# Performance work log

Hardware: AMD Instinct MI355X
Metric: run time of the kernel (lower is better)

Reference implementation:

```python
import jax, jax.numpy as jnp
import numpy as np

C = 256
CQK = C // 8  # reduction_ratio = 8


def setup_inputs() -> dict:
    key = jax.random.key(0)
    ks = jax.random.split(key, 8)
    B, H, W = 8, 64, 64
    x = jax.random.normal(ks[0], (B, C, H, W), dtype=jnp.float32)
    s_in = 1.0 / np.sqrt(C)
    Wq = jax.random.normal(ks[1], (CQK, C), dtype=jnp.float32) * s_in
    bq = jax.random.normal(ks[2], (CQK,), dtype=jnp.float32) * 0.01
    Wk = jax.random.normal(ks[3], (CQK, C), dtype=jnp.float32) * s_in
    bk = jax.random.normal(ks[4], (CQK,), dtype=jnp.float32) * 0.01
    Wv = jax.random.normal(ks[5], (C, C), dtype=jnp.float32) * s_in
    bv = jax.random.normal(ks[6], (C,), dtype=jnp.float32) * 0.01
    gamma = jax.random.normal(ks[7], (1,), dtype=jnp.float32) * 0.1
    return {"x": x, "Wq": Wq, "bq": bq, "Wk": Wk, "bk": bk,
            "Wv": Wv, "bv": bv, "gamma": gamma}


def reference(x, Wq, bq, Wk, bk, Wv, bv, gamma):
    B, Cc, H, W = x.shape
    N = H * W
    xf = x.reshape(B, Cc, N)  # [B, C, N]
    # 1x1 convs == per-pixel linear maps over channels
    q = jnp.einsum('qc,bcn->bnq', Wq, xf) + bq            # [B, N, Cqk]
    k = jnp.einsum('kc,bcn->bkn', Wk, xf) + bk[None, :, None]  # [B, Cqk, N]
    v = jnp.einsum('vc,bcn->bvn', Wv, xf) + bv[None, :, None]  # [B, C, N]
    # unscaled attention scores, softmax over keys (last dim)
    scores = jax.nn.softmax(jnp.einsum('bnq,bqm->bnm', q, k), axis=-1)  # [B, N, N]
    # out[b,c,n] = sum_m v[b,c,m] * scores[b,n,m]  (torch: value @ scores^T)
    attn = jnp.einsum('bvm,bnm->bvn', v, scores)          # [B, C, N]
    out = gamma[0] * attn.reshape(B, Cc, H, W) + x
    return out
```

## Files before the change

### kernel.cpp

```cpp
#include <hip/hip_runtime.h>

static constexpr int B_   = 8;
static constexpr int C_   = 256;
static constexpr int CQK_ = 32;
static constexpr int N_   = 4096;

typedef __attribute__((ext_vector_type(4)))  float f32x4;
typedef __attribute__((ext_vector_type(16))) float f32x16;
typedef __attribute__((ext_vector_type(8)))  short short8;
typedef __attribute__((ext_vector_type(2)))  unsigned int u32x2;
typedef unsigned short ushort_t;

__device__ inline unsigned short f2bf(float f) {
    unsigned u = __float_as_uint(f);
    return (unsigned short)((u + 0x7FFFu + ((u >> 16) & 1u)) >> 16);
}
__device__ inline unsigned packbf(float lo, float hi) {
    return (unsigned)f2bf(lo) | ((unsigned)f2bf(hi) << 16);
}
__device__ inline unsigned cvtpk(float lo, float hi) {
    unsigned r;
    asm("v_cvt_pk_bf16_f32 %0, %1, %2" : "=v"(r) : "v"(lo), "v"(hi));
    return r;
}
__device__ inline float vexp2(float x) {
    float r;
    asm("v_exp_f32 %0, %1" : "=v"(r) : "v"(x));
    return r;
}
__device__ inline void plswap(unsigned& a, unsigned& b) {
    asm("v_permlane32_swap_b32 %0, %1" : "+v"(a), "+v"(b));
}

__device__ inline int swzbits(int m) {
    return ((m & 3) << 5) | (((m >> 3) & 1) << 4);
}

template <int OFF>
__device__ inline u32x2 tr8(unsigned a) {
    u32x2 d;
    asm volatile("ds_read_b64_tr_b16 %0, %1 offset:%2"
                 : "=v"(d) : "v"(a), "i"(OFF));
    return d;
}

__device__ inline short8 mk8(u32x2 lo, u32x2 hi) {
    union { unsigned u[4]; short8 s; } v;
    v.u[0] = lo.x; v.u[1] = lo.y; v.u[2] = hi.x; v.u[3] = hi.y;
    return v.s;
}
__device__ inline short8 mk8u(unsigned a, unsigned b, unsigned c, unsigned d) {
    union { unsigned u[4]; short8 s; } v;
    v.u[0] = a; v.u[1] = b; v.u[2] = c; v.u[3] = d;
    return v.s;
}

__global__ __launch_bounds__(256) void prep_kernel(
    const float* __restrict__ Wq, const float* __restrict__ bq,
    const float* __restrict__ Wk, const float* __restrict__ bk,
    const float* __restrict__ Wv, const float* __restrict__ bv,
    ushort_t* __restrict__ Wall, float* __restrict__ ball)
{
    const int r = blockIdx.x;
    const int t = threadIdx.x;
    const float LOG2E = 1.4426950408889634f;
    const float* src;
    float bsrc, sc;
    if (r < 32)      { src = Wq + (size_t)r * C_;        bsrc = bq[r];      sc = LOG2E; }
    else if (r < 64) { src = Wk + (size_t)(r - 32) * C_; bsrc = bk[r - 32]; sc = 1.0f; }
    else             { src = Wv + (size_t)(r - 64) * C_; bsrc = bv[r - 64]; sc = 1.0f; }
    Wall[(size_t)r * C_ + t] = f2bf(src[t] * sc);
    if (t == 0) ball[r] = bsrc * sc;
}

__global__ __launch_bounds__(256) void proj_kernel(
    const float* __restrict__ x,
    const ushort_t* __restrict__ Wall, const float* __restrict__ ball,
    ushort_t* __restrict__ Qb, ushort_t* __restrict__ Kb, ushort_t* __restrict__ Vt)
{
    __shared__ __align__(16) unsigned char xs[C_ * 128];
    typedef __attribute__((address_space(3))) unsigned char lds_byte;
    const unsigned sbase = (unsigned)(size_t)(lds_byte*)xs;

    const int b  = blockIdx.x & 7;
    const int n0 = (blockIdx.x >> 3) << 6;
    const int t  = threadIdx.x;

    {
        const int cst = t >> 4;
        const int n4  = (t & 15) << 2;
        const float* xb = x + (size_t)b * C_ * N_ + n0;
        #pragma unroll
        for (int i = 0; i < 16; ++i) {
            const int c = 16 * i + cst;
            float4 v = *(const float4*)(xb + (size_t)c * N_ + n4);
            u32x2 pk;
            pk.x = packbf(v.x, v.y);
            pk.y = packbf(v.z, v.w);
            *(u32x2*)(xs + c * 128 + ((n4 * 2) ^ swzbits(c))) = pk;
        }
    }
    __syncthreads();

    const int l  = t & 63, w = t >> 6;
    const int li = l & 15, g = l >> 4;
    const int rr = li >> 2, ss = l & 3;
    const int swz_tr = (rr << 5) | ((g & 1) << 4);

    f32x4 acc[5][4];
    #pragma unroll
    for (int i = 0; i < 5; ++i)
        #pragma unroll
        for (int j = 0; j < 4; ++j) acc[i][j] = (f32x4){0.f, 0.f, 0.f, 0.f};

    #pragma unroll 2
    for (int kg = 0; kg < 8; ++kg) {
        u32x2 pb[4][2];
        #pragma unroll
        for (int jn = 0; jn < 4; ++jn) {
            unsigned a = sbase + (32 * kg + 8 * g + rr) * 128
                       + ((32 * jn + 8 * ss) ^ swz_tr);
            pb[jn][0] = tr8<0>(a);
            pb[jn][1] = tr8<512>(a);
        }
        short8 af[5];
        #pragma unroll
        for (int tm = 0; tm < 5; ++tm)
            af[tm] = *(const short8*)(Wall + (size_t)(16 * (4 * tm + w) + li) * C_
                                      + 32 * kg + 8 * g);
        asm volatile("s_waitcnt lgkmcnt(0)" ::: "memory");
        __builtin_amdgcn_sched_barrier(0);
        #pragma unroll
        for (int jn = 0; jn < 4; ++jn) {
            short8 Bf = mk8(pb[jn][0], pb[jn][1]);
            acc[0][jn] = __builtin_amdgcn_mfma_f32_16x16x32_bf16(
                             af[0], Bf, acc[0][jn], 0, 0, 0);
            #pragma unroll
            for (int tm = 1; tm < 5; ++tm)
                acc[tm][jn] = __builtin_amdgcn_mfma_f32_16x16x32_bf16(
                                  Bf, af[tm], acc[tm][jn], 0, 0, 0);
        }
    }

    {
        const int oc0 = 16 * w + 4 * g;
        float4 bias = *(const float4*)(ball + oc0);
        ushort_t* dst = (w < 2) ? Qb : Kb;
        const int col = (w < 2) ? oc0 : (oc0 - 32);
        #pragma unroll
        for (int jn = 0; jn < 4; ++jn) {
            const int n = n0 + 16 * jn + li;
            f32x4 a = acc[0][jn];
            u32x2 pk;
            pk.x = packbf(a[0] + bias.x, a[1] + bias.y);
            pk.y = packbf(a[2] + bias.z, a[3] + bias.w);
            *(u32x2*)(dst + (size_t)(b * N_ + n) * CQK_ + col) = pk;
        }
    }
    #pragma unroll
    for (int tm = 1; tm < 5; ++tm) {
        const int c  = 16 * (4 * tm + w) + li - 64;
        const float bc = ball[64 + c];
        const int ch = c >> 7;
        const int cl = c & 127;
        const int X  = (c & 3) ^ ((c >> 2) & 3);
        char* qbase = (char*)Vt + ((size_t)(b * 64 + (n0 >> 6)) * 4 + 2 * ch) * 8192
                    + cl * 64;
        #pragma unroll
        for (int jn = 0; jn < 4; ++jn) {
            const int mp = 16 * jn + 4 * g;
            const int mh = mp >> 5;
            const int jg = (mp & 31) >> 3;
            f32x4 a = acc[tm][jn];
            u32x2 pk;
            pk.x = packbf(a[0] + bc, a[1] + bc);
            pk.y = packbf(a[2] + bc, a[3] + bc);
            *(u32x2*)(qbase + mh * 8192 + 16 * (jg ^ X) + 8 * (g & 1)) = pk;
        }
    }
}

__global__ __launch_bounds__(256, 2) void attn_kernel(
    const float* __restrict__ x,
    const ushort_t* __restrict__ Qb, const ushort_t* __restrict__ Kb,
    const ushort_t* __restrict__ Vt,
    const float* __restrict__ gamma, float* __restrict__ out)
{
    __shared__ __align__(16) unsigned char smem[66560];

    const int b   = blockIdx.x & 7;
    const int n0  = (blockIdx.x >> 3) << 6;
    const int t   = threadIdx.x;
    const int l   = t & 63, w = t >> 6;
    const int l31 = l & 31, h2 = l >> 5;
    const int mh  = w & 1,  ch = w >> 1;
    const int sxv = ((l31 & 3) ^ ((l31 >> 2) & 3)) << 4;
    unsigned char* wlds = smem + w * 16384;
    float* rstab = (float*)(smem + 65536);

    short8 qfv[2][2];
    #pragma unroll
    for (int jq = 0; jq < 2; ++jq)
        #pragma unroll
        for (int kh = 0; kh < 2; ++kh)
            qfv[jq][kh] = *(const short8*)(Qb
                + (size_t)(b * N_ + n0 + 32 * jq + l31) * CQK_ + 16 * kh + 8 * h2);

    f32x16 acc[2][4];
    #pragma unroll
    for (int i = 0; i < 2; ++i)
        #pragma unroll
        for (int j = 0; j < 4; ++j)
            #pragma unroll
            for (int e = 0; e < 16; ++e) acc[i][j][e] = 0.f;
    f32x16 zf16;
    #pragma unroll
    for (int e = 0; e < 16; ++e) zf16[e] = 0.f;
    float rs[2] = {0.f, 0.f};

    const ushort_t* Kbb = Kb + (size_t)(b * N_) * CQK_;
    const char* Vgb = (const char*)Vt + (size_t)b * 64 * 32768
                    + (2 * ch + mh) * 8192;

    short8 kfA[2], kfB[2];

    #pragma unroll
    for (int kh = 0; kh < 2; ++kh)
        kfA[kh] = *(const short8*)(Kbb + (size_t)(32 * mh + l31) * CQK_
                                   + 16 * kh + 8 * h2);
    #pragma unroll
    for (int i = 0; i < 8; ++i)
        __builtin_amdgcn_global_load_lds(
            (const __attribute__((address_space(1))) unsigned int*)(Vgb + l * 16 + i * 1024),
            (__attribute__((address_space(3))) unsigned int*)(wlds + l * 16 + i * 1024),
            16, 0, 0);

#define CHUNK_BODY(CH, KFC, KFN)                                                \
    {                                                                           \
        const int chn = ((CH) + 1) & 63;                                        \
                                              \
        _Pragma("unroll")                                                       \
        for (int kh = 0; kh < 2; ++kh)                                          \
            KFN[kh] = *(const short8*)(Kbb                                      \
                + (size_t)(64 * chn + 32 * mh + l31) * CQK_ + 16 * kh + 8 * h2);\
                    \
        {                                                                       \
            const char* gsrc = Vgb + (size_t)chn * 32768 + l * 16;              \
            unsigned char* ldst = wlds + (((CH) + 1) & 1) * 8192 + l * 16;      \
            _Pragma("unroll")                                                   \
            for (int i = 0; i < 8; ++i)                                         \
                __builtin_amdgcn_global_load_lds(                               \
                    (const __attribute__((address_space(1))) unsigned int*)(gsrc + i * 1024), \
                    (__attribute__((address_space(3))) unsigned int*)(ldst + i * 1024), \
                    16, 0, 0);                                                  \
        }                                                                       \
                     \
        unsigned paw[2][2][4];                                                  \
        _Pragma("unroll")                                                       \
        for (int jq = 0; jq < 2; ++jq) {                                        \
            f32x16 sv = __builtin_amdgcn_mfma_f32_32x32x16_bf16(                \
                            KFC[0], qfv[jq][0], zf16, 0, 0, 0);                 \
            sv = __builtin_amdgcn_mfma_f32_32x32x16_bf16(                       \
                     KFC[1], qfv[jq][1], sv, 0, 0, 0);                          \
            float ev[16];                                                       \
            _Pragma("unroll")                                                   \
            for (int e = 0; e < 16; ++e) ev[e] = vexp2(sv[e]);                  \
            rs[jq] += (((ev[0] + ev[1]) + (ev[2] + ev[3]))                      \
                     + ((ev[4] + ev[5]) + (ev[6] + ev[7])))                     \
                    + (((ev[8] + ev[9]) + (ev[10] + ev[11]))                    \
                     + ((ev[12] + ev[13]) + (ev[14] + ev[15])));                \
            unsigned u0 = cvtpk(ev[0], ev[1]),   u1 = cvtpk(ev[2], ev[3]);      \
            unsigned u2 = cvtpk(ev[4], ev[5]),   u3 = cvtpk(ev[6], ev[7]);      \
            unsigned u4 = cvtpk(ev[8], ev[9]),   u5 = cvtpk(ev[10], ev[11]);    \
            unsigned u6 = cvtpk(ev[12], ev[13]), u7 = cvtpk(ev[14], ev[15]);    \
            plswap(u0, u2); plswap(u1, u3);                                     \
            plswap(u4, u6); plswap(u5, u7);                                     \
            paw[jq][0][0] = u0; paw[jq][0][1] = u1;                             \
            paw[jq][0][2] = u2; paw[jq][0][3] = u3;                             \
            paw[jq][1][0] = u4; paw[jq][1][1] = u5;                             \
            paw[jq][1][2] = u6; paw[jq][1][3] = u7;                             \
        }                                                                       \
                \
        asm volatile("s_waitcnt vmcnt(10)" ::: "memory");                       \
               \
        {                                                                       \
            const unsigned char* vb = wlds + ((CH) & 1) * 8192;                 \
            _Pragma("unroll")                                                   \
            for (int s = 0; s < 2; ++s) {                                       \
                short8 vv[4];                                                   \
                _Pragma("unroll")                                               \
                for (int jc = 0; jc < 4; ++jc)                                  \
                    vv[jc] = *(const short8*)(vb + (32 * jc + l31) * 64         \
                                   + ((32 * s + 16 * h2) ^ sxv));               \
                _Pragma("unroll")                                               \
                for (int jq = 0; jq < 2; ++jq) {                                \
                    short8 A = mk8u(paw[jq][s][0], paw[jq][s][1],               \
                                    paw[jq][s][2], paw[jq][s][3]);              \
                    _Pragma("unroll")                                           \
                    for (int jc = 0; jc < 4; ++jc)                              \
                        acc[jq][jc] = __builtin_amdgcn_mfma_f32_32x32x16_bf16(  \
                                          A, vv[jc], acc[jq][jc], 0, 0, 0);     \
                }                                                               \
            }                                                                   \
        }                                                                       \
    }

    for (int mc = 0; mc < 64; mc += 2) {
        CHUNK_BODY(mc,     kfA, kfB)
        CHUNK_BODY(mc + 1, kfB, kfA)
    }
#undef CHUNK_BODY

    #pragma unroll
    for (int jq = 0; jq < 2; ++jq)
        rs[jq] += __shfl_xor(rs[jq], 32, 64);
    if (l < 32) {
        rstab[(w * 2 + 0) * 32 + l31] = rs[0];
        rstab[(w * 2 + 1) * 32 + l31] = rs[1];
    }
    asm volatile("s_waitcnt vmcnt(0)" ::: "memory");
    __syncthreads();

    if (mh == 1) {
        float* dst = (float*)(smem + ch * 32768);
        #pragma unroll
        for (int jq = 0; jq < 2; ++jq)
            #pragma unroll
            for (int jc = 0; jc < 4; ++jc) {
                float* tb = dst + (jq * 4 + jc) * 1024 + l * 16;
                #pragma unroll
                for (int e4 = 0; e4 < 4; ++e4) {
                    f32x4 p;
                    p[0] = acc[jq][jc][4 * e4 + 0];
                    p[1] = acc[jq][jc][4 * e4 + 1];
                    p[2] = acc[jq][jc][4 * e4 + 2];
                    p[3] = acc[jq][jc][4 * e4 + 3];
                    *(f32x4*)(tb + 4 * (e4 ^ (l & 3))) = p;
                }
            }
    }
    __syncthreads();

    if (mh == 0) {
        const float* src = (const float*)(smem + ch * 32768);
        #pragma unroll
        for (int jq = 0; jq < 2; ++jq)
            #pragma unroll
            for (int jc = 0; jc < 4; ++jc) {
                const float* tb = src + (jq * 4 + jc) * 1024 + l * 16;
                #pragma unroll
                for (int e4 = 0; e4 < 4; ++e4) {
                    f32x4 p = *(const f32x4*)(tb + 4 * (e4 ^ (l & 3)));
                    acc[jq][jc][4 * e4 + 0] += p[0];
                    acc[jq][jc][4 * e4 + 1] += p[1];
                    acc[jq][jc][4 * e4 + 2] += p[2];
                    acc[jq][jc][4 * e4 + 3] += p[3];
                }
            }
        const float gm = gamma[0];
        #pragma unroll
        for (int jq = 0; jq < 2; ++jq)
            #pragma unroll
            for (int rg = 0; rg < 4; ++rg) {
                f32x4 s0 = *(const f32x4*)(rstab + (w * 2 + jq) * 32
                                           + 8 * rg + 4 * h2);
                f32x4 s1 = *(const f32x4*)(rstab + ((w + 1) * 2 + jq) * 32
                                           + 8 * rg + 4 * h2);
                float i0 = 1.0f / (s0[0] + s1[0]);
                float i1 = 1.0f / (s0[1] + s1[1]);
                float i2 = 1.0f / (s0[2] + s1[2]);
                float i3 = 1.0f / (s0[3] + s1[3]);
                const int n = n0 + 32 * jq + 8 * rg + 4 * h2;
                #pragma unroll
                for (int jc = 0; jc < 4; ++jc) {
                    const int c = 128 * ch + 32 * jc + l31;
                    const size_t rowoff = (size_t)(b * C_ + c) * N_ + n;
                    float4 xv = *(const float4*)(x + rowoff);
                    float4 o;
                    o.x = gm * acc[jq][jc][4 * rg + 0] * i0 + xv.x;
                    o.y = gm * acc[jq][jc][4 * rg + 1] * i1 + xv.y;
                    o.z = gm * acc[jq][jc][4 * rg + 2] * i2 + xv.z;
                    o.w = gm * acc[jq][jc][4 * rg + 3] * i3 + xv.w;
                    *(float4*)(out + rowoff) = o;
                }
            }
    }
}

extern "C" void kernel_launch(void* const* d_in, const int* in_sizes, int n_in,
                              void* d_out, int out_size, void* d_ws, size_t ws_size,
                              hipStream_t stream)
{
    const float* x     = (const float*)d_in[0];
    const float* Wq    = (const float*)d_in[1];
    const float* bq    = (const float*)d_in[2];
    const float* Wk    = (const float*)d_in[3];
    const float* bk    = (const float*)d_in[4];
    const float* Wv    = (const float*)d_in[5];
    const float* bv    = (const float*)d_in[6];
    const float* gamma = (const float*)d_in[7];
    float* out = (float*)d_out;

    ushort_t* ws = (ushort_t*)d_ws;
    ushort_t* Qb   = ws;
    ushort_t* Kb   = Qb + (size_t)B_ * N_ * CQK_;
    ushort_t* Vt   = Kb + (size_t)B_ * N_ * CQK_;
    ushort_t* Wall = Vt + (size_t)B_ * C_ * N_;
    float*    ball = (float*)(Wall + (size_t)320 * C_);

    prep_kernel<<<320, 256, 0, stream>>>(Wq, bq, Wk, bk, Wv, bv, Wall, ball);
    proj_kernel<<<B_ * (N_ / 64), 256, 0, stream>>>(x, Wall, ball, Qb, Kb, Vt);
    attn_kernel<<<B_ * (N_ / 64), 256, 0, stream>>>(x, Qb, Kb, Vt, gamma, out);
}
```

Before: 138.0 us.

## Software-pipeline QK softmax one chunk ahead of PV MFMAs

```diff
diff --git a/kernel.cpp b/kernel.cpp
--- a/kernel.cpp
+++ b/kernel.cpp
@@ -223,30 +223,57 @@
                     + (2 * ch + mh) * 8192;
 
     short8 kfA[2], kfB[2];
-
-    #pragma unroll
-    for (int kh = 0; kh < 2; ++kh)
-        kfA[kh] = *(const short8*)(Kbb + (size_t)(32 * mh + l31) * CQK_
-                                   + 16 * kh + 8 * h2);
-    #pragma unroll
-    for (int i = 0; i < 8; ++i)
-        __builtin_amdgcn_global_load_lds(
-            (const __attribute__((address_space(1))) unsigned int*)(Vgb + l * 16 + i * 1024),
-            (__attribute__((address_space(3))) unsigned int*)(wlds + l * 16 + i * 1024),
-            16, 0, 0);
-
-#define CHUNK_BODY(CH, KFC, KFN)                                                \
+    unsigned pA[2][2][4], pB[2][2][4];
+
+#define QK_JQ(JQ, KQ, PN)                                                       \
     {                                                                           \
-        const int chn = ((CH) + 1) & 63;                                        \
-                                              \
+        f32x16 sv = __builtin_amdgcn_mfma_f32_32x32x16_bf16(                    \
+                        KQ[0], qfv[JQ][0], zf16, 0, 0, 0);                      \
+        sv = __builtin_amdgcn_mfma_f32_32x32x16_bf16(                           \
+                 KQ[1], qfv[JQ][1], sv, 0, 0, 0);                               \
+        _Pragma("unroll")                                                       \
+        for (int s = 0; s < 2; ++s) {                                           \
+            float e0 = vexp2(sv[8*s+0]), e1 = vexp2(sv[8*s+1]);                 \
+            float e2 = vexp2(sv[8*s+2]), e3 = vexp2(sv[8*s+3]);                 \
+            float e4 = vexp2(sv[8*s+4]), e5 = vexp2(sv[8*s+5]);                 \
+            float e6 = vexp2(sv[8*s+6]), e7 = vexp2(sv[8*s+7]);                 \
+            rs[JQ] += ((e0 + e1) + (e2 + e3)) + ((e4 + e5) + (e6 + e7));        \
+            unsigned u0 = cvtpk(e0, e1), u1 = cvtpk(e2, e3);                    \
+            unsigned u2 = cvtpk(e4, e5), u3 = cvtpk(e6, e7);                    \
+            plswap(u0, u2); plswap(u1, u3);                                     \
+            PN[JQ][s][0] = u0; PN[JQ][s][1] = u1;                               \
+            PN[JQ][s][2] = u2; PN[JQ][s][3] = u3;                               \
+        }                                                                       \
+    }
+
+#define PV_S(S, PC, VB)                                                         \
+    {                                                                           \
+        short8 A0 = mk8u(PC[0][S][0], PC[0][S][1], PC[0][S][2], PC[0][S][3]);   \
+        short8 A1 = mk8u(PC[1][S][0], PC[1][S][1], PC[1][S][2], PC[1][S][3]);   \
+        _Pragma("unroll")                                                       \
+        for (int jc = 0; jc < 4; ++jc) {                                        \
+            short8 vv = *(const short8*)((VB) + (32 * jc + l31) * 64            \
+                           + ((32 * (S) + 16 * h2) ^ sxv));                     \
+            acc[0][jc] = __builtin_amdgcn_mfma_f32_32x32x16_bf16(               \
+                             A0, vv, acc[0][jc], 0, 0, 0);                      \
+            acc[1][jc] = __builtin_amdgcn_mfma_f32_32x32x16_bf16(               \
+                             A1, vv, acc[1][jc], 0, 0, 0);                      \
+        }                                                                       \
+    }
+
+#define BODY(N, KQ, KL, PC, PN)                                                 \
+    {                                                                           \
+        const int chk = ((N) + 2) & 63;                                         \
+        const int chd = ((N) + 1) & 63;                                         \
+                         \
         _Pragma("unroll")                                                       \
         for (int kh = 0; kh < 2; ++kh)                                          \
-            KFN[kh] = *(const short8*)(Kbb                                      \
-                + (size_t)(64 * chn + 32 * mh + l31) * CQK_ + 16 * kh + 8 * h2);\
-                    \
+            KL[kh] = *(const short8*)(Kbb                                       \
+                + (size_t)(64 * chk + 32 * mh + l31) * CQK_ + 16 * kh + 8 * h2);\
+                                  \
         {                                                                       \
-            const char* gsrc = Vgb + (size_t)chn * 32768 + l * 16;              \
-            unsigned char* ldst = wlds + (((CH) + 1) & 1) * 8192 + l * 16;      \
+            const char* gsrc = Vgb + (size_t)chd * 32768 + l * 16;              \
+            unsigned char* ldst = wlds + (chd & 1) * 8192 + l * 16;             \
             _Pragma("unroll")                                                   \
             for (int i = 0; i < 8; ++i)                                         \
                 __builtin_amdgcn_global_load_lds(                               \
@@ -254,62 +281,52 @@
                     (__attribute__((address_space(3))) unsigned int*)(ldst + i * 1024), \
                     16, 0, 0);                                                  \
         }                                                                       \
-                     \
-        unsigned paw[2][2][4];                                                  \
-        _Pragma("unroll")                                                       \
-        for (int jq = 0; jq < 2; ++jq) {                                        \
-            f32x16 sv = __builtin_amdgcn_mfma_f32_32x32x16_bf16(                \
-                            KFC[0], qfv[jq][0], zf16, 0, 0, 0);                 \
-            sv = __builtin_amdgcn_mfma_f32_32x32x16_bf16(                       \
-                     KFC[1], qfv[jq][1], sv, 0, 0, 0);                          \
-            float ev[16];                                                       \
-            _Pragma("unroll")                                                   \
-            for (int e = 0; e < 16; ++e) ev[e] = vexp2(sv[e]);                  \
-            rs[jq] += (((ev[0] + ev[1]) + (ev[2] + ev[3]))                      \
-                     + ((ev[4] + ev[5]) + (ev[6] + ev[7])))                     \
-                    + (((ev[8] + ev[9]) + (ev[10] + ev[11]))                    \
-                     + ((ev[12] + ev[13]) + (ev[14] + ev[15])));                \
-            unsigned u0 = cvtpk(ev[0], ev[1]),   u1 = cvtpk(ev[2], ev[3]);      \
-            unsigned u2 = cvtpk(ev[4], ev[5]),   u3 = cvtpk(ev[6], ev[7]);      \
-            unsigned u4 = cvtpk(ev[8], ev[9]),   u5 = cvtpk(ev[10], ev[11]);    \
-            unsigned u6 = cvtpk(ev[12], ev[13]), u7 = cvtpk(ev[14], ev[15]);    \
-            plswap(u0, u2); plswap(u1, u3);                                     \
-            plswap(u4, u6); plswap(u5, u7);                                     \
-            paw[jq][0][0] = u0; paw[jq][0][1] = u1;                             \
-            paw[jq][0][2] = u2; paw[jq][0][3] = u3;                             \
-            paw[jq][1][0] = u4; paw[jq][1][1] = u5;                             \
-            paw[jq][1][2] = u6; paw[jq][1][3] = u7;                             \
-        }                                                                       \
                 \
         asm volatile("s_waitcnt vmcnt(10)" ::: "memory");                       \
-               \
+                         \
+        __builtin_amdgcn_s_setprio(1);                                          \
         {                                                                       \
-            const unsigned char* vb = wlds + ((CH) & 1) * 8192;                 \
-            _Pragma("unroll")                                                   \
-            for (int s = 0; s < 2; ++s) {                                       \
-                short8 vv[4];                                                   \
-                _Pragma("unroll")                                               \
-                for (int jc = 0; jc < 4; ++jc)                                  \
-                    vv[jc] = *(const short8*)(vb + (32 * jc + l31) * 64         \
-                                   + ((32 * s + 16 * h2) ^ sxv));               \
-                _Pragma("unroll")                                               \
-                for (int jq = 0; jq < 2; ++jq) {                                \
-                    short8 A = mk8u(paw[jq][s][0], paw[jq][s][1],               \
-                                    paw[jq][s][2], paw[jq][s][3]);              \
-                    _Pragma("unroll")                                           \
-                    for (int jc = 0; jc < 4; ++jc)                              \
-                        acc[jq][jc] = __builtin_amdgcn_mfma_f32_32x32x16_bf16(  \
-                                          A, vv[jc], acc[jq][jc], 0, 0, 0);     \
-                }                                                               \
-            }                                                                   \
+            const unsigned char* vb = wlds + ((N) & 1) * 8192;                  \
+            QK_JQ(0, KQ, PN)                                                    \
+            PV_S(0, PC, vb)                                                     \
+            QK_JQ(1, KQ, PN)                                                    \
+            PV_S(1, PC, vb)                                                     \
         }                                                                       \
-    }
-
-    for (int mc = 0; mc < 64; mc += 2) {
-        CHUNK_BODY(mc,     kfA, kfB)
-        CHUNK_BODY(mc + 1, kfB, kfA)
-    }
-#undef CHUNK_BODY
+        __builtin_amdgcn_s_setprio(0);                                          \
+    }
+
+    #pragma unroll
+    for (int kh = 0; kh < 2; ++kh) {
+        kfA[kh] = *(const short8*)(Kbb + (size_t)(32 * mh + l31) * CQK_
+                                   + 16 * kh + 8 * h2);
+        kfB[kh] = *(const short8*)(Kbb + (size_t)(64 + 32 * mh + l31) * CQK_
+                                   + 16 * kh + 8 * h2);
+    }
+    #pragma unroll
+    for (int i = 0; i < 8; ++i)
+        __builtin_amdgcn_global_load_lds(
+            (const __attribute__((address_space(1))) unsigned int*)(Vgb + l * 16 + i * 1024),
+            (__attribute__((address_space(3))) unsigned int*)(wlds + l * 16 + i * 1024),
+            16, 0, 0);
+    asm volatile("s_waitcnt vmcnt(10)" ::: "memory");
+    QK_JQ(0, kfA, pA)
+    QK_JQ(1, kfA, pA)
+
+    for (int mc = 0; mc < 62; mc += 2) {
+        BODY(mc,     kfB, kfA, pA, pB)
+        BODY(mc + 1, kfA, kfB, pB, pA)
+    }
+    BODY(62, kfB, kfA, pA, pB)
+
+    asm volatile("s_waitcnt vmcnt(0)" ::: "memory");
+    {
+        const unsigned char* vb = wlds + 8192;
+        PV_S(0, pB, vb)
+        PV_S(1, pB, vb)
+    }
+#undef BODY
+#undef PV_S
+#undef QK_JQ
 
     #pragma unroll
     for (int jq = 0; jq < 2; ++jq)
@@ -318,7 +335,6 @@
         rstab[(w * 2 + 0) * 32 + l31] = rs[0];
         rstab[(w * 2 + 1) * 32 + l31] = rs[1];
     }
-    asm volatile("s_waitcnt vmcnt(0)" ::: "memory");
     __syncthreads();
 
     if (mh == 1) {
```

New measurement: 130.5 us. 1.06x faster.
